# Kernel tuning notes

Measured on AMD Instinct MI355X. Metric: run time of the kernel, lower is better.

The kernel has to match this reference:

```python
import jax, jax.numpy as jnp
import numpy as np

N = 50000
E = 800000
C = 64
NEG_SLOPE = 0.2


def gat_conv(x, edge_index, W, att_src, att_dst, bias, heads, out_ch):
    """PyG GATConv forward (concat=True, add_self_loops=True).
    x: [N, in], edge_index: [2, E] (row0=src j, row1=dst i),
    W: [in, heads*out_ch], att_src/att_dst: [heads, out_ch], bias: [heads*out_ch].
    """
    n = x.shape[0]
    loop = jnp.arange(n, dtype=edge_index.dtype)
    src = jnp.concatenate([edge_index[0], loop])
    dst = jnp.concatenate([edge_index[1], loop])

    xl = (x @ W).reshape(n, heads, out_ch)            # [N, H, F]
    a_src = jnp.einsum('nhf,hf->nh', xl, att_src)      # [N, H]
    a_dst = jnp.einsum('nhf,hf->nh', xl, att_dst)      # [N, H]

    alpha = jax.nn.leaky_relu(a_src[src] + a_dst[dst], NEG_SLOPE)  # [E', H]
    # segment softmax over incoming edges of each destination node
    amax = jax.ops.segment_max(alpha, dst, num_segments=n)
    alpha = jnp.exp(alpha - amax[dst])
    denom = jax.ops.segment_sum(alpha, dst, num_segments=n)
    alpha = alpha / denom[dst]

    # gather source features, weight, scatter-add to destinations
    msg = xl[src] * alpha[:, :, None]                  # [E', H, F]
    out = jax.ops.segment_sum(msg, dst, num_segments=n)  # [N, H, F]
    return out.reshape(n, heads * out_ch) + bias


def setup_inputs() -> dict:
    key = jax.random.key(0)
    ks = jax.random.split(key, 12)
    x = jax.random.normal(ks[0], (N, C), dtype=jnp.float32)
    undirected = jax.random.randint(ks[1], (2, E), 0, N, dtype=jnp.int32)
    directed = jax.random.randint(ks[2], (2, E), 0, N, dtype=jnp.int32)

    s1 = 1.0 / np.sqrt(C)
    s2 = 1.0 / np.sqrt(2 * C)
    W1 = jax.random.normal(ks[3], (C, 2 * C), dtype=jnp.float32) * s1
    att_src1 = jax.random.normal(ks[4], (2, C), dtype=jnp.float32) * s1
    att_dst1 = jax.random.normal(ks[5], (2, C), dtype=jnp.float32) * s1
    b1 = jnp.zeros((2 * C,), dtype=jnp.float32)

    W2 = jax.random.normal(ks[6], (2 * C, 4 * C), dtype=jnp.float32) * s2
    att_src2 = jax.random.normal(ks[7], (2, 2 * C), dtype=jnp.float32) * s2
    att_dst2 = jax.random.normal(ks[8], (2, 2 * C), dtype=jnp.float32) * s2
    b2 = jnp.zeros((4 * C,), dtype=jnp.float32)

    return {
        'x': x,
        'undirected_edges_small': undirected,
        'directed_edges_small': directed,
        'W1': W1, 'att_src1': att_src1, 'att_dst1': att_dst1, 'b1': b1,
        'W2': W2, 'att_src2': att_src2, 'att_dst2': att_dst2, 'b2': b2,
    }


def reference(x, undirected_edges_small, directed_edges_small,
              W1, att_src1, att_dst1, b1,
              W2, att_src2, att_dst2, b2):
    h = gat_conv(x, undirected_edges_small, W1, att_src1, att_dst1, b1,
                 heads=2, out_ch=C)            # [N, 2C]
    out = gat_conv(h, directed_edges_small, W2, att_src2, att_dst2, b2,
                   heads=2, out_ch=2 * C)      # [N, 4C]
    return out
```

## Files before the change

kernel.cpp:

```cpp
#include <hip/hip_runtime.h>
#include <stdint.h>

#define N_NODES 50000
#define N_EDGES 800000
#define CAP 64
#define NBUCK 400
#define BSZ 125
#define BCAP 2816

typedef __attribute__((ext_vector_type(8))) short bf16x8;
typedef __attribute__((ext_vector_type(4))) float f32x4;

__device__ __forceinline__ float b2f_bits(unsigned int lo16) {
    union { unsigned int i; float f; } v; v.i = lo16 << 16; return v.f;
}
__device__ __forceinline__ unsigned short f2b(float f) {
    union { float f; unsigned int i; } v; v.f = f;
    unsigned int x = v.i;
    return (unsigned short)((x + 0x7fffu + ((x >> 16) & 1u)) >> 16);
}
__device__ __forceinline__ void split2(float v, unsigned short& h, unsigned short& l) {
    h = f2b(v);
    l = f2b(v - b2f_bits(h));
}

__global__ __launch_bounds__(256) void proj_kernel(
    const float* __restrict__ W1, const float* __restrict__ as1, const float* __restrict__ ad1,
    const float* __restrict__ b1,
    const float* __restrict__ W2, const float* __restrict__ as2, const float* __restrict__ ad2,
    float* __restrict__ P1, float* __restrict__ q2, float* __restrict__ cs)
{
    __shared__ float p2[4 * 128];
    for (int i = threadIdx.x; i < 4 * 128; i += 256) {
        const int t = i >> 7, c = i & 127;
        const int h = t & 1;
        const float* att = (t < 2) ? as2 : ad2;
        float s = 0.f;
        for (int cc = 0; cc < 128; ++cc)
            s += att[h * 128 + cc] * W2[(size_t)c * 256 + h * 128 + cc];
        p2[i] = s;
    }
    {
        const int t = threadIdx.x >> 6, k = threadIdx.x & 63;
        const int h = t & 1;
        const float* att = (t < 2) ? as1 : ad1;
        float s = 0.f;
        for (int c = 0; c < 64; ++c)
            s += att[h * 64 + c] * W1[(size_t)k * 128 + h * 64 + c];
        P1[t * 64 + k] = s;
    }
    __syncthreads();
    for (int i = threadIdx.x; i < 4 * 128; i += 256) {
        const int t = i >> 7, j = i & 127;
        const int hc = j >> 6, k = j & 63;
        float s = 0.f;
        for (int c = 0; c < 64; ++c)
            s += W1[(size_t)k * 128 + hc * 64 + c] * p2[t * 128 + hc * 64 + c];
        q2[i] = s;
    }
    if (threadIdx.x < 4) {
        const int t = threadIdx.x;
        float s = 0.f;
        for (int c = 0; c < 128; ++c) s += b1[c] * p2[t * 128 + c];
        cs[t] = s;
    }
}

__global__ __launch_bounds__(256) void prep1_kernel(
    const float* __restrict__ X, const float* __restrict__ P1,
    unsigned short* __restrict__ Xh,
    float* __restrict__ a_src, float* __restrict__ a_dst, int n)
{
    const int node = (blockIdx.x * 256 + threadIdx.x) >> 4;
    const int sl = threadIdx.x & 15;
    if (node >= n) return;
    const float4 v = *(const float4*)(X + (size_t)node * 64 + sl * 4);
    ushort4 hv;
    hv.x = f2b(v.x); hv.y = f2b(v.y); hv.z = f2b(v.z); hv.w = f2b(v.w);
    *(ushort4*)(Xh + (size_t)node * 64 + sl * 4) = hv;
    float d[4];
#pragma unroll
    for (int t = 0; t < 4; ++t) {
        const float* pp = P1 + t * 64 + sl * 4;
        d[t] = v.x * pp[0] + v.y * pp[1] + v.z * pp[2] + v.w * pp[3];
    }
#pragma unroll
    for (int o = 1; o < 16; o <<= 1)
#pragma unroll
        for (int t = 0; t < 4; ++t) d[t] += __shfl_xor(d[t], o);
    if (sl == 0) {
        *(float2*)(a_src + node * 2) = make_float2(d[0], d[1]);
        *(float2*)(a_dst + node * 2) = make_float2(d[2], d[3]);
    }
}

__global__ __launch_bounds__(256) void splitWT_kernel(
    const float* __restrict__ W,
    unsigned short* __restrict__ WhT, unsigned short* __restrict__ WlT, int K, int N)
{
    const int i = blockIdx.x * 256 + threadIdx.x;
    if (i >= N * K) return;
    const int n = i / K, k = i % K;
    const float v = W[(size_t)k * N + n];
    unsigned short h, l;
    split2(v, h, l);
    WhT[i] = h; WlT[i] = l;
}

__global__ __launch_bounds__(256) void bucket_kernel(
    const int* __restrict__ e1, const int* __restrict__ e2, int ne,
    int* __restrict__ gcur, unsigned int* __restrict__ stage)
{
    const int layer = blockIdx.x & 1;
    const int bslot = blockIdx.x >> 1;
    const int nbl = gridDim.x >> 1;
    const int* __restrict__ eix = layer ? e2 : e1;
    int* cur = gcur + layer * NBUCK;
    unsigned int* __restrict__ stg = stage + (size_t)layer * NBUCK * BCAP;

    __shared__ int cnt_lds[NBUCK];
    __shared__ int base_lds[NBUCK];
    constexpr int EPT = 16;
    constexpr int CHUNK = 256 * EPT;

    for (int base = bslot * CHUNK; base < ne; base += nbl * CHUNK) {
        for (int i = threadIdx.x; i < NBUCK; i += 256) cnt_lds[i] = 0;
        __syncthreads();

        unsigned int rec[EPT];
        int bk[EPT];
#pragma unroll
        for (int i = 0; i < EPT; ++i) {
            const int e = base + i * 256 + threadIdx.x;
            bk[i] = -1;
            if (e < ne) {
                const int s = eix[e];
                const int d = eix[ne + e];
                if ((unsigned)d < (unsigned)N_NODES) {
                    const int b = d / BSZ;
                    bk[i] = b;
                    rec[i] = (unsigned)s | ((unsigned)(d - b * BSZ) << 16);
                    atomicAdd(&cnt_lds[b], 1);
                }
            }
        }
        __syncthreads();
        for (int i = threadIdx.x; i < NBUCK; i += 256) {
            const int c = cnt_lds[i];
            base_lds[i] = c ? atomicAdd(&cur[i], c) : 0;
            cnt_lds[i] = 0;
        }
        __syncthreads();
#pragma unroll
        for (int i = 0; i < EPT; ++i) {
            if (bk[i] >= 0) {
                const int idx = base_lds[bk[i]] + atomicAdd(&cnt_lds[bk[i]], 1);
                if (idx < BCAP) stg[(size_t)bk[i] * BCAP + idx] = rec[i];
            }
        }
        __syncthreads();
    }
}

__global__ __launch_bounds__(256) void place_kernel(
    const unsigned int* __restrict__ stage, const int* __restrict__ gcur,
    int* __restrict__ cnt1, int* __restrict__ cnt2,
    int* __restrict__ ss1, int* __restrict__ ss2)
{
    const int layer = blockIdx.x & 1;
    const int bucket = blockIdx.x >> 1;
    int m = gcur[layer * NBUCK + bucket];
    m = m < BCAP ? m : BCAP;
    const unsigned int* __restrict__ stg =
        stage + ((size_t)(layer * NBUCK + bucket)) * BCAP;
    int* __restrict__ cnt = layer ? cnt2 : cnt1;
    int* __restrict__ ss  = layer ? ss2 : ss1;
    const int d0 = bucket * BSZ;

    __shared__ int c_lds[BSZ];
    __shared__ __align__(16) unsigned int img[BSZ * CAP];

    for (int i = threadIdx.x; i < BSZ; i += 256) c_lds[i] = 0;
    __syncthreads();

    for (int i = threadIdx.x; i < m; i += 256) {
        const unsigned int v = stg[i];
        const int dr = (int)(v >> 16);
        const int slot = atomicAdd(&c_lds[dr], 1);
        if (slot < CAP) img[dr * CAP + slot] = v & 0xffffu;
    }
    __syncthreads();

    uint4* dst4 = (uint4*)(ss + (size_t)d0 * CAP);
    const uint4* src4 = (const uint4*)img;
    constexpr int NV4 = BSZ * CAP / 4;
    for (int i = threadIdx.x; i < NV4; i += 256) dst4[i] = src4[i];
    for (int i = threadIdx.x; i < BSZ; i += 256) {
        const int c = c_lds[i];
        cnt[d0 + i] = c < CAP ? c : CAP;
    }
}

__global__ __launch_bounds__(256) void agg1_kernel(
    const unsigned short* __restrict__ XH, const float* __restrict__ X,
    const float* __restrict__ a_src, const float* __restrict__ a_dst,
    const int* __restrict__ cnt, const int* __restrict__ bins,
    unsigned short* __restrict__ AH, unsigned short* __restrict__ AL, int n)
{
    const int node = (blockIdx.x * 256 + threadIdx.x) >> 6;
    const int lane = threadIdx.x & 63;
    if (node >= n) return;
    const int hl = lane & 15;
    const int sub = lane >> 4;

    const int s = node * CAP;
    int deg = cnt[node]; deg = deg < CAP ? deg : CAP;
    const int e = s + deg;
    const float2 ad = *(const float2*)(a_dst + node * 2);

    float acc0[4] = {0.f, 0.f, 0.f, 0.f}, acc1[4] = {0.f, 0.f, 0.f, 0.f};
    float den0 = 0.f, den1 = 0.f;

    int p = s;
    for (; p + 8 <= e; p += 8) {
        int j[2];
        j[0] = bins[p + sub];
        j[1] = bins[p + 4 + sub];
        float2 A[2];
        A[0] = *(const float2*)(a_src + j[0] * 2);
        A[1] = *(const float2*)(a_src + j[1] * 2);
        uint2 u[2];
        u[0] = *(const uint2*)(XH + (size_t)j[0] * 64 + hl * 4);
        u[1] = *(const uint2*)(XH + (size_t)j[1] * 64 + hl * 4);
#pragma unroll
        for (int g = 0; g < 2; ++g) {
            float l0 = A[g].x + ad.x; l0 = l0 > 0.f ? l0 : 0.2f * l0;
            float l1 = A[g].y + ad.y; l1 = l1 > 0.f ? l1 : 0.2f * l1;
            const float w0 = __expf(l0), w1 = __expf(l1);
            den0 += w0; den1 += w1;
            float f[4];
            f[0] = b2f_bits(u[g].x & 0xffffu); f[1] = b2f_bits(u[g].x >> 16);
            f[2] = b2f_bits(u[g].y & 0xffffu); f[3] = b2f_bits(u[g].y >> 16);
#pragma unroll
            for (int k = 0; k < 4; ++k) { acc0[k] += w0 * f[k]; acc1[k] += w1 * f[k]; }
        }
    }
    for (; p < e; p += 4) {
        const int pos = p + sub;
        const int pc = pos < e ? pos : e - 1;
        const int j = bins[pc];
        const float2 A = *(const float2*)(a_src + j * 2);
        const uint2 u = *(const uint2*)(XH + (size_t)j * 64 + hl * 4);
        float l0 = A.x + ad.x; l0 = l0 > 0.f ? l0 : 0.2f * l0;
        float l1 = A.y + ad.y; l1 = l1 > 0.f ? l1 : 0.2f * l1;
        float w0 = __expf(l0), w1 = __expf(l1);
        if (pos >= e) { w0 = 0.f; w1 = 0.f; }
        den0 += w0; den1 += w1;
        float f[4];
        f[0] = b2f_bits(u.x & 0xffffu); f[1] = b2f_bits(u.x >> 16);
        f[2] = b2f_bits(u.y & 0xffffu); f[3] = b2f_bits(u.y >> 16);
#pragma unroll
        for (int k = 0; k < 4; ++k) { acc0[k] += w0 * f[k]; acc1[k] += w1 * f[k]; }
    }
    if (sub == 0) {
        const float2 A = *(const float2*)(a_src + node * 2);
        const float4 v = *(const float4*)(X + (size_t)node * 64 + hl * 4);
        float l0 = A.x + ad.x; l0 = l0 > 0.f ? l0 : 0.2f * l0;
        float l1 = A.y + ad.y; l1 = l1 > 0.f ? l1 : 0.2f * l1;
        const float w0 = __expf(l0), w1 = __expf(l1);
        den0 += w0; den1 += w1;
        acc0[0] += w0 * v.x; acc0[1] += w0 * v.y; acc0[2] += w0 * v.z; acc0[3] += w0 * v.w;
        acc1[0] += w1 * v.x; acc1[1] += w1 * v.y; acc1[2] += w1 * v.z; acc1[3] += w1 * v.w;
    }
#pragma unroll
    for (int o = 16; o < 64; o <<= 1) {
        den0 += __shfl_xor(den0, o); den1 += __shfl_xor(den1, o);
#pragma unroll
        for (int k = 0; k < 4; ++k) {
            acc0[k] += __shfl_xor(acc0[k], o);
            acc1[k] += __shfl_xor(acc1[k], o);
        }
    }
    if (lane < 32) {
        const int head = lane >> 4;
        float vv[4];
        if (head) {
            const float inv = 1.f / den1;
            vv[0] = acc1[0] * inv; vv[1] = acc1[1] * inv;
            vv[2] = acc1[2] * inv; vv[3] = acc1[3] * inv;
        } else {
            const float inv = 1.f / den0;
            vv[0] = acc0[0] * inv; vv[1] = acc0[1] * inv;
            vv[2] = acc0[2] * inv; vv[3] = acc0[3] * inv;
        }
        ushort4 hv, lv;
        split2(vv[0], hv.x, lv.x); split2(vv[1], hv.y, lv.y);
        split2(vv[2], hv.z, lv.z); split2(vv[3], hv.w, lv.w);
        const size_t off = (size_t)head * N_NODES * 64 + (size_t)node * 64 + hl * 4;
        *(ushort4*)(AH + off) = hv;
        *(ushort4*)(AL + off) = lv;
    }
}

__global__ __launch_bounds__(256) void att2_kernel(
    const unsigned short* __restrict__ A1H, const unsigned short* __restrict__ A1L,
    const float* __restrict__ q2, const float* __restrict__ cs,
    float* __restrict__ a_src, float* __restrict__ a_dst, int n)
{
    const int node = (blockIdx.x * 256 + threadIdx.x) >> 6;
    const int lane = threadIdx.x & 63;
    if (node >= n) return;
    const int hc = lane >> 5;
    const int k2 = (lane & 31) * 2;
    const size_t off = (size_t)hc * N_NODES * 64 + (size_t)node * 64 + k2;
    const unsigned int uh = *(const unsigned int*)(A1H + off);
    const unsigned int ul = *(const unsigned int*)(A1L + off);
    const float v0 = b2f_bits(uh & 0xffffu) + b2f_bits(ul & 0xffffu);
    const float v1 = b2f_bits(uh >> 16) + b2f_bits(ul >> 16);
    const int j = hc * 64 + k2;
    float d[4];
#pragma unroll
    for (int t = 0; t < 4; ++t)
        d[t] = v0 * q2[t * 128 + j] + v1 * q2[t * 128 + j + 1];
#pragma unroll
    for (int o = 1; o < 64; o <<= 1)
#pragma unroll
        for (int t = 0; t < 4; ++t) d[t] += __shfl_xor(d[t], o);
    if (lane == 0) {
        *(float2*)(a_src + node * 2) = make_float2(d[0] + cs[0], d[1] + cs[1]);
        *(float2*)(a_dst + node * 2) = make_float2(d[2] + cs[2], d[3] + cs[3]);
    }
}

__global__ __launch_bounds__(256) void agg2_kernel(
    const unsigned short* __restrict__ HH, const unsigned short* __restrict__ HL,
    const float* __restrict__ a_src, const float* __restrict__ a_dst,
    const int* __restrict__ cnt, const int* __restrict__ bins,
    unsigned short* __restrict__ AH, unsigned short* __restrict__ AL, int n)
{
    const int node = (blockIdx.x * 256 + threadIdx.x) >> 6;
    const int lane = threadIdx.x & 63;
    if (node >= n) return;
    const int hl = lane & 31;
    const int sub = lane >> 5;

    const int s = node * CAP;
    int deg = cnt[node]; deg = deg < CAP ? deg : CAP;
    const int e = s + deg;
    const float2 ad = *(const float2*)(a_dst + node * 2);

    float acc0[4] = {0.f, 0.f, 0.f, 0.f}, acc1[4] = {0.f, 0.f, 0.f, 0.f};
    float den0 = 0.f, den1 = 0.f;

    int p = s;
    for (; p + 8 <= e; p += 8) {
        int j[4];
#pragma unroll
        for (int g = 0; g < 4; ++g) j[g] = bins[p + g * 2 + sub];
        float2 A[4];
#pragma unroll
        for (int g = 0; g < 4; ++g) A[g] = *(const float2*)(a_src + j[g] * 2);
        uint2 u[4];
#pragma unroll
        for (int g = 0; g < 4; ++g)
            u[g] = *(const uint2*)(HH + (size_t)j[g] * 128 + hl * 4);
#pragma unroll
        for (int g = 0; g < 4; ++g) {
            float l0 = A[g].x + ad.x; l0 = l0 > 0.f ? l0 : 0.2f * l0;
            float l1 = A[g].y + ad.y; l1 = l1 > 0.f ? l1 : 0.2f * l1;
            const float w0 = __expf(l0), w1 = __expf(l1);
            den0 += w0; den1 += w1;
            float f[4];
            f[0] = b2f_bits(u[g].x & 0xffffu); f[1] = b2f_bits(u[g].x >> 16);
            f[2] = b2f_bits(u[g].y & 0xffffu); f[3] = b2f_bits(u[g].y >> 16);
#pragma unroll
            for (int k = 0; k < 4; ++k) { acc0[k] += w0 * f[k]; acc1[k] += w1 * f[k]; }
        }
    }
    for (; p < e; p += 2) {
        const int pos = p + sub;
        const int pc = pos < e ? pos : e - 1;
        const int j = bins[pc];
        const float2 A = *(const float2*)(a_src + j * 2);
        const uint2 u = *(const uint2*)(HH + (size_t)j * 128 + hl * 4);
        float l0 = A.x + ad.x; l0 = l0 > 0.f ? l0 : 0.2f * l0;
        float l1 = A.y + ad.y; l1 = l1 > 0.f ? l1 : 0.2f * l1;
        float w0 = __expf(l0), w1 = __expf(l1);
        if (pos >= e) { w0 = 0.f; w1 = 0.f; }
        den0 += w0; den1 += w1;
        float f[4];
        f[0] = b2f_bits(u.x & 0xffffu); f[1] = b2f_bits(u.x >> 16);
        f[2] = b2f_bits(u.y & 0xffffu); f[3] = b2f_bits(u.y >> 16);
#pragma unroll
        for (int k = 0; k < 4; ++k) { acc0[k] += w0 * f[k]; acc1[k] += w1 * f[k]; }
    }
    if (sub == 0) {
        const float2 A = *(const float2*)(a_src + node * 2);
        const uint2 uh = *(const uint2*)(HH + (size_t)node * 128 + hl * 4);
        const uint2 ul = *(const uint2*)(HL + (size_t)node * 128 + hl * 4);
        float l0 = A.x + ad.x; l0 = l0 > 0.f ? l0 : 0.2f * l0;
        float l1 = A.y + ad.y; l1 = l1 > 0.f ? l1 : 0.2f * l1;
        const float w0 = __expf(l0), w1 = __expf(l1);
        den0 += w0; den1 += w1;
        float f[4];
        f[0] = b2f_bits(uh.x & 0xffffu) + b2f_bits(ul.x & 0xffffu);
        f[1] = b2f_bits(uh.x >> 16) + b2f_bits(ul.x >> 16);
        f[2] = b2f_bits(uh.y & 0xffffu) + b2f_bits(ul.y & 0xffffu);
        f[3] = b2f_bits(uh.y >> 16) + b2f_bits(ul.y >> 16);
#pragma unroll
        for (int k = 0; k < 4; ++k) { acc0[k] += w0 * f[k]; acc1[k] += w1 * f[k]; }
    }
    den0 += __shfl_xor(den0, 32); den1 += __shfl_xor(den1, 32);
#pragma unroll
    for (int k = 0; k < 4; ++k) {
        acc0[k] += __shfl_xor(acc0[k], 32);
        acc1[k] += __shfl_xor(acc1[k], 32);
    }
    {
        const int head = sub;
        float vv[4];
        if (head) {
            const float inv = 1.f / den1;
            vv[0] = acc1[0] * inv; vv[1] = acc1[1] * inv;
            vv[2] = acc1[2] * inv; vv[3] = acc1[3] * inv;
        } else {
            const float inv = 1.f / den0;
            vv[0] = acc0[0] * inv; vv[1] = acc0[1] * inv;
            vv[2] = acc0[2] * inv; vv[3] = acc0[3] * inv;
        }
        ushort4 hv, lv;
        split2(vv[0], hv.x, lv.x); split2(vv[1], hv.y, lv.y);
        split2(vv[2], hv.z, lv.z); split2(vv[3], hv.w, lv.w);
        const size_t off = (size_t)head * N_NODES * 128 + (size_t)node * 128 + hl * 4;
        *(ushort4*)(AH + off) = hv;
        *(ushort4*)(AL + off) = lv;
    }
}

__global__ __launch_bounds__(512) void gemm_h_kernel(
    const unsigned short* __restrict__ AH, const unsigned short* __restrict__ AL,
    const unsigned short* __restrict__ WTh, const unsigned short* __restrict__ WTl,
    const float* __restrict__ b1,
    unsigned short* __restrict__ HH, unsigned short* __restrict__ HL, int M)
{
    constexpr int K = 64, KC = 2;
    const int wave = threadIdx.x >> 6;
    const int lane = threadIdx.x & 63;
    const int head = wave >> 2;
    const int c0 = (wave & 3) * 16;
    const int lr = lane & 15;
    const int lk = (lane >> 4) * 8;
    const int colg = head * 64 + c0 + ((lane >> 4) << 2);

    bf16x8 awh[KC], awl[KC];
    {
        const unsigned short* wr  = WTh + (size_t)(head * 64 + c0 + lr) * K + lk;
        const unsigned short* wr2 = WTl + (size_t)(head * 64 + c0 + lr) * K + lk;
#pragma unroll
        for (int c = 0; c < KC; ++c) {
            awh[c] = *(const bf16x8*)(wr + c * 32);
            awl[c] = *(const bf16x8*)(wr2 + c * 32);
        }
    }
    const float4 bias = *(const float4*)(b1 + colg);
    const unsigned short* XhB = AH + (size_t)head * M * 64;
    const unsigned short* XlB = AL + (size_t)head * M * 64;

    auto loadB = [&](bf16x8 (&bh)[KC], bf16x8 (&bl)[KC], int sidx) {
        const unsigned short* xr  = XhB + (size_t)(sidx * 16 + lr) * 64 + lk;
        const unsigned short* xr2 = XlB + (size_t)(sidx * 16 + lr) * 64 + lk;
#pragma unroll
        for (int c = 0; c < KC; ++c) {
            bh[c] = *(const bf16x8*)(xr + c * 32);
            bl[c] = *(const bf16x8*)(xr2 + c * 32);
        }
    };
    auto compute = [&](bf16x8 (&bh)[KC], bf16x8 (&bl)[KC], int sidx) {
        f32x4 acc = {0.f, 0.f, 0.f, 0.f};
#pragma unroll
        for (int c = 0; c < KC; ++c)
            acc = __builtin_amdgcn_mfma_f32_16x16x32_bf16(awh[c], bh[c], acc, 0, 0, 0);
#pragma unroll
        for (int c = 0; c < KC; ++c)
            acc = __builtin_amdgcn_mfma_f32_16x16x32_bf16(awh[c], bl[c], acc, 0, 0, 0);
#pragma unroll
        for (int c = 0; c < KC; ++c)
            acc = __builtin_amdgcn_mfma_f32_16x16x32_bf16(awl[c], bh[c], acc, 0, 0, 0);
        ushort4 hv, lv;
        split2(acc[0] + bias.x, hv.x, lv.x); split2(acc[1] + bias.y, hv.y, lv.y);
        split2(acc[2] + bias.z, hv.z, lv.z); split2(acc[3] + bias.w, hv.w, lv.w);
        const size_t o = (size_t)(sidx * 16 + lr) * 128 + colg;
        *(ushort4*)(HH + o) = hv;
        *(ushort4*)(HL + o) = lv;
    };

    const int NSTRIP = M / 16;
    const int nb = gridDim.x;
    int s = blockIdx.x;
    bf16x8 b0h[KC], b0l[KC], b1h_[KC], b1l_[KC];
    if (s < NSTRIP) loadB(b0h, b0l, s);
    while (s < NSTRIP) {
        const int sn = s + nb;
        if (sn < NSTRIP) loadB(b1h_, b1l_, sn);
        compute(b0h, b0l, s);
        if (sn >= NSTRIP) break;
        const int sn2 = sn + nb;
        if (sn2 < NSTRIP) loadB(b0h, b0l, sn2);
        compute(b1h_, b1l_, sn);
        s = sn2;
    }
}

__global__ __launch_bounds__(512) void gemm_out_kernel(
    const unsigned short* __restrict__ AH, const unsigned short* __restrict__ AL,
    const unsigned short* __restrict__ WTh, const unsigned short* __restrict__ WTl,
    const float* __restrict__ b2,
    float* __restrict__ OUT, int M)
{
    constexpr int K = 128, KC = 4, CT = 2;
    const int wave = threadIdx.x >> 6;
    const int lane = threadIdx.x & 63;
    const int head = wave >> 2;
    const int c0 = (wave & 3) * 32;
    const int lr = lane & 15;
    const int lk = (lane >> 4) * 8;

    bf16x8 awh[CT][KC], awl[CT][KC];
    float4 bias[CT];
    int colg[CT];
#pragma unroll
    for (int t = 0; t < CT; ++t) {
        const unsigned short* wr  = WTh + (size_t)(head * 128 + c0 + t * 16 + lr) * K + lk;
        const unsigned short* wr2 = WTl + (size_t)(head * 128 + c0 + t * 16 + lr) * K + lk;
#pragma unroll
        for (int c = 0; c < KC; ++c) {
            awh[t][c] = *(const bf16x8*)(wr + c * 32);
            awl[t][c] = *(const bf16x8*)(wr2 + c * 32);
        }
        colg[t] = head * 128 + c0 + t * 16 + ((lane >> 4) << 2);
        bias[t] = *(const float4*)(b2 + colg[t]);
    }
    const unsigned short* XhB = AH + (size_t)head * M * 128;
    const unsigned short* XlB = AL + (size_t)head * M * 128;

    auto loadB = [&](bf16x8 (&bh)[KC], bf16x8 (&bl)[KC], int sidx) {
        const unsigned short* xr  = XhB + (size_t)(sidx * 16 + lr) * 128 + lk;
        const unsigned short* xr2 = XlB + (size_t)(sidx * 16 + lr) * 128 + lk;
#pragma unroll
        for (int c = 0; c < KC; ++c) {
            bh[c] = *(const bf16x8*)(xr + c * 32);
            bl[c] = *(const bf16x8*)(xr2 + c * 32);
        }
    };
    auto compute = [&](bf16x8 (&bh)[KC], bf16x8 (&bl)[KC], int sidx) {
#pragma unroll
        for (int t = 0; t < CT; ++t) {
            f32x4 acc = {0.f, 0.f, 0.f, 0.f};
#pragma unroll
            for (int c = 0; c < KC; ++c)
                acc = __builtin_amdgcn_mfma_f32_16x16x32_bf16(awh[t][c], bh[c], acc, 0, 0, 0);
#pragma unroll
            for (int c = 0; c < KC; ++c)
                acc = __builtin_amdgcn_mfma_f32_16x16x32_bf16(awh[t][c], bl[c], acc, 0, 0, 0);
#pragma unroll
            for (int c = 0; c < KC; ++c)
                acc = __builtin_amdgcn_mfma_f32_16x16x32_bf16(awl[t][c], bh[c], acc, 0, 0, 0);
            float4 o;
            o.x = acc[0] + bias[t].x; o.y = acc[1] + bias[t].y;
            o.z = acc[2] + bias[t].z; o.w = acc[3] + bias[t].w;
            *(float4*)(OUT + (size_t)(sidx * 16 + lr) * 256 + colg[t]) = o;
        }
    };

    const int NSTRIP = M / 16;
    const int nb = gridDim.x;
    int s = blockIdx.x;
    bf16x8 b0h[KC], b0l[KC], b1h_[KC], b1l_[KC];
    if (s < NSTRIP) loadB(b0h, b0l, s);
    while (s < NSTRIP) {
        const int sn = s + nb;
        if (sn < NSTRIP) loadB(b1h_, b1l_, sn);
        compute(b0h, b0l, s);
        if (sn >= NSTRIP) break;
        const int sn2 = sn + nb;
        if (sn2 < NSTRIP) loadB(b0h, b0l, sn2);
        compute(b1h_, b1l_, sn);
        s = sn2;
    }
}

extern "C" void kernel_launch(void* const* d_in, const int* in_sizes, int n_in,
                              void* d_out, int out_size, void* d_ws, size_t ws_size,
                              hipStream_t stream)
{
    const int N = N_NODES, E = N_EDGES;

    const float* x   = (const float*)d_in[0];
    const int*   und = (const int*)d_in[1];
    const int*   dir = (const int*)d_in[2];
    const float* W1  = (const float*)d_in[3];
    const float* as1 = (const float*)d_in[4];
    const float* ad1 = (const float*)d_in[5];
    const float* b1  = (const float*)d_in[6];
    const float* W2  = (const float*)d_in[7];
    const float* as2 = (const float*)d_in[8];
    const float* ad2 = (const float*)d_in[9];
    const float* b2  = (const float*)d_in[10];

    char* p = (char*)d_ws;
    auto alloc = [&](size_t bytes) {
        char* r = p;
        p += (bytes + 255) & ~(size_t)255;
        return r;
    };
    unsigned short* agg2h = (unsigned short*)alloc((size_t)2 * N * 128 * 2);
    unsigned short* agg2l = (unsigned short*)alloc((size_t)2 * N * 128 * 2);
    unsigned short* hlbuf = (unsigned short*)alloc((size_t)N * 128 * 2);
    int*   ss1   = (int*)alloc((size_t)N * CAP * 4);
    int*   ss2   = (int*)alloc((size_t)N * CAP * 4);
    float* a_src1 = (float*)alloc((size_t)N * 2 * 4);
    float* a_dst1 = (float*)alloc((size_t)N * 2 * 4);
    float* a_src2 = (float*)alloc((size_t)N * 2 * 4);
    float* a_dst2 = (float*)alloc((size_t)N * 2 * 4);
    int*   cnts  = (int*)alloc(((size_t)2 * N + 2 * NBUCK) * 4);
    unsigned short* w1th = (unsigned short*)alloc((size_t)128 * 64 * 2);
    unsigned short* w1tl = (unsigned short*)alloc((size_t)128 * 64 * 2);
    unsigned short* w2th = (unsigned short*)alloc((size_t)256 * 128 * 2);
    unsigned short* w2tl = (unsigned short*)alloc((size_t)256 * 128 * 2);
    float* P1d = (float*)alloc(4 * 64 * 4);
    float* q2d = (float*)alloc(4 * 128 * 4);
    float* csd = (float*)alloc(4 * 4);
    int* cnt1 = cnts, * cnt2 = cnts + N, * gcur = cnts + 2 * N;

    unsigned int* stage = (unsigned int*)agg2h;
    unsigned short* hhbuf = (unsigned short*)ss1;
    unsigned short* x1h   = (unsigned short*)d_out;
    unsigned short* agg1h = (unsigned short*)d_out + (size_t)N * 64;
    unsigned short* agg1l = (unsigned short*)d_out + (size_t)N * 64 + (size_t)N * 128;

    const int WB = (N * 64) / 256;

    proj_kernel<<<1, 256, 0, stream>>>(W1, as1, ad1, b1, W2, as2, ad2, P1d, q2d, csd);
    hipMemsetAsync(gcur, 0, (size_t)2 * NBUCK * 4, stream);
    bucket_kernel<<<2 * 196, 256, 0, stream>>>(und, dir, E, gcur, stage);
    place_kernel<<<2 * NBUCK, 256, 0, stream>>>(stage, gcur, cnt1, cnt2, ss1, ss2);
    prep1_kernel<<<(N * 16) / 256, 256, 0, stream>>>(x, P1d, x1h, a_src1, a_dst1, N);
    splitWT_kernel<<<(128 * 64 + 255) / 256, 256, 0, stream>>>(W1, w1th, w1tl, 64, 128);
    splitWT_kernel<<<(256 * 128 + 255) / 256, 256, 0, stream>>>(W2, w2th, w2tl, 128, 256);

    agg1_kernel<<<WB, 256, 0, stream>>>(x1h, x, a_src1, a_dst1, cnt1, ss1, agg1h, agg1l, N);
    gemm_h_kernel<<<768, 512, 0, stream>>>(agg1h, agg1l, w1th, w1tl, b1, hhbuf, hlbuf, N);
    att2_kernel<<<WB, 256, 0, stream>>>(agg1h, agg1l, q2d, csd, a_src2, a_dst2, N);

    agg2_kernel<<<WB, 256, 0, stream>>>(hhbuf, hlbuf, a_src2, a_dst2, cnt2, ss2, agg2h, agg2l, N);
    gemm_out_kernel<<<512, 512, 0, stream>>>(agg2h, agg2l, w2th, w2tl, b2, (float*)d_out, N);
}
```

Before: 297.1 us.

## Fuse layer-2 attention logits into gemm_h, widen aggregation loads, merge W prep

The separate att2_kernel is removed. The layer-2 attention projections are now computed inside gemm_h_kernel from the A tiles already held in registers, and accumulated into a zeroed buffer with atomicAdd. The cs constant is folded into the a_dst term in agg2. Both aggregation kernels switch from 8-byte to 16-byte gather loads with 8 features per lane and drop the unrolled main loop. The two weight-split kernels are merged into one launch. The changes aim to cut a full pass over agg1 and a launch, at the cost of atomics, an extra memset and more register pressure in the GEMM.

```diff
diff --git a/kernel.cpp b/kernel.cpp
--- a/kernel.cpp
+++ b/kernel.cpp
@@ -22,6 +22,21 @@
 __device__ __forceinline__ void split2(float v, unsigned short& h, unsigned short& l) {
     h = f2b(v);
     l = f2b(v - b2f_bits(h));
+}
+__device__ __forceinline__ void unpack8(const uint4 u, float* f) {
+    f[0] = b2f_bits(u.x & 0xffffu); f[1] = b2f_bits(u.x >> 16);
+    f[2] = b2f_bits(u.y & 0xffffu); f[3] = b2f_bits(u.y >> 16);
+    f[4] = b2f_bits(u.z & 0xffffu); f[5] = b2f_bits(u.z >> 16);
+    f[6] = b2f_bits(u.w & 0xffffu); f[7] = b2f_bits(u.w >> 16);
+}
+__device__ __forceinline__ void pack8hl(const float* v, uint4& H, uint4& L) {
+    unsigned short h[8], l[8];
+#pragma unroll
+    for (int k = 0; k < 8; ++k) split2(v[k], h[k], l[k]);
+    H.x = h[0] | ((unsigned)h[1] << 16); H.y = h[2] | ((unsigned)h[3] << 16);
+    H.z = h[4] | ((unsigned)h[5] << 16); H.w = h[6] | ((unsigned)h[7] << 16);
+    L.x = l[0] | ((unsigned)l[1] << 16); L.y = l[2] | ((unsigned)l[3] << 16);
+    L.z = l[4] | ((unsigned)l[5] << 16); L.w = l[6] | ((unsigned)l[7] << 16);
 }
 
 __global__ __launch_bounds__(256) void proj_kernel(
@@ -94,17 +109,25 @@
     }
 }
 
-__global__ __launch_bounds__(256) void splitWT_kernel(
-    const float* __restrict__ W,
-    unsigned short* __restrict__ WhT, unsigned short* __restrict__ WlT, int K, int N)
-{
-    const int i = blockIdx.x * 256 + threadIdx.x;
-    if (i >= N * K) return;
-    const int n = i / K, k = i % K;
-    const float v = W[(size_t)k * N + n];
-    unsigned short h, l;
-    split2(v, h, l);
-    WhT[i] = h; WlT[i] = l;
+__global__ __launch_bounds__(256) void prepW_kernel(
+    const float* __restrict__ W1, const float* __restrict__ W2,
+    unsigned short* __restrict__ w1h, unsigned short* __restrict__ w1l,
+    unsigned short* __restrict__ w2h, unsigned short* __restrict__ w2l)
+{
+    const int bid = blockIdx.x;
+    if (bid < 128) {
+        const int i = bid * 256 + threadIdx.x;
+        const int n = i >> 7, k = i & 127;
+        unsigned short h, l;
+        split2(W2[(size_t)k * 256 + n], h, l);
+        w2h[i] = h; w2l[i] = l;
+    } else {
+        const int i = (bid - 128) * 256 + threadIdx.x;
+        const int n = i >> 6, k = i & 63;
+        unsigned short h, l;
+        split2(W1[(size_t)k * 128 + n], h, l);
+        w1h[i] = h; w1l[i] = l;
+    }
 }
 
 __global__ __launch_bounds__(256) void bucket_kernel(
@@ -210,238 +233,154 @@
     const int node = (blockIdx.x * 256 + threadIdx.x) >> 6;
     const int lane = threadIdx.x & 63;
     if (node >= n) return;
-    const int hl = lane & 15;
-    const int sub = lane >> 4;
+    const int hl = lane & 7;
+    const int sub = lane >> 3;
 
     const int s = node * CAP;
     int deg = cnt[node]; deg = deg < CAP ? deg : CAP;
     const int e = s + deg;
     const float2 ad = *(const float2*)(a_dst + node * 2);
 
-    float acc0[4] = {0.f, 0.f, 0.f, 0.f}, acc1[4] = {0.f, 0.f, 0.f, 0.f};
+    float acc0[8] = {0.f,0.f,0.f,0.f,0.f,0.f,0.f,0.f};
+    float acc1[8] = {0.f,0.f,0.f,0.f,0.f,0.f,0.f,0.f};
     float den0 = 0.f, den1 = 0.f;
 
-    int p = s;
-    for (; p + 8 <= e; p += 8) {
-        int j[2];
-        j[0] = bins[p + sub];
-        j[1] = bins[p + 4 + sub];
-        float2 A[2];
-        A[0] = *(const float2*)(a_src + j[0] * 2);
-        A[1] = *(const float2*)(a_src + j[1] * 2);
-        uint2 u[2];
-        u[0] = *(const uint2*)(XH + (size_t)j[0] * 64 + hl * 4);
-        u[1] = *(const uint2*)(XH + (size_t)j[1] * 64 + hl * 4);
-#pragma unroll
-        for (int g = 0; g < 2; ++g) {
-            float l0 = A[g].x + ad.x; l0 = l0 > 0.f ? l0 : 0.2f * l0;
-            float l1 = A[g].y + ad.y; l1 = l1 > 0.f ? l1 : 0.2f * l1;
-            const float w0 = __expf(l0), w1 = __expf(l1);
-            den0 += w0; den1 += w1;
-            float f[4];
-            f[0] = b2f_bits(u[g].x & 0xffffu); f[1] = b2f_bits(u[g].x >> 16);
-            f[2] = b2f_bits(u[g].y & 0xffffu); f[3] = b2f_bits(u[g].y >> 16);
-#pragma unroll
-            for (int k = 0; k < 4; ++k) { acc0[k] += w0 * f[k]; acc1[k] += w1 * f[k]; }
-        }
-    }
-    for (; p < e; p += 4) {
+    for (int p = s; p < e; p += 8) {
         const int pos = p + sub;
         const int pc = pos < e ? pos : e - 1;
         const int j = bins[pc];
         const float2 A = *(const float2*)(a_src + j * 2);
-        const uint2 u = *(const uint2*)(XH + (size_t)j * 64 + hl * 4);
+        const uint4 u = *(const uint4*)(XH + (size_t)j * 64 + hl * 8);
         float l0 = A.x + ad.x; l0 = l0 > 0.f ? l0 : 0.2f * l0;
         float l1 = A.y + ad.y; l1 = l1 > 0.f ? l1 : 0.2f * l1;
         float w0 = __expf(l0), w1 = __expf(l1);
         if (pos >= e) { w0 = 0.f; w1 = 0.f; }
         den0 += w0; den1 += w1;
-        float f[4];
-        f[0] = b2f_bits(u.x & 0xffffu); f[1] = b2f_bits(u.x >> 16);
-        f[2] = b2f_bits(u.y & 0xffffu); f[3] = b2f_bits(u.y >> 16);
-#pragma unroll
-        for (int k = 0; k < 4; ++k) { acc0[k] += w0 * f[k]; acc1[k] += w1 * f[k]; }
+        float f[8]; unpack8(u, f);
+#pragma unroll
+        for (int k = 0; k < 8; ++k) { acc0[k] += w0 * f[k]; acc1[k] += w1 * f[k]; }
     }
     if (sub == 0) {
         const float2 A = *(const float2*)(a_src + node * 2);
-        const float4 v = *(const float4*)(X + (size_t)node * 64 + hl * 4);
+        const float4 va = *(const float4*)(X + (size_t)node * 64 + hl * 8);
+        const float4 vb = *(const float4*)(X + (size_t)node * 64 + hl * 8 + 4);
         float l0 = A.x + ad.x; l0 = l0 > 0.f ? l0 : 0.2f * l0;
         float l1 = A.y + ad.y; l1 = l1 > 0.f ? l1 : 0.2f * l1;
         const float w0 = __expf(l0), w1 = __expf(l1);
         den0 += w0; den1 += w1;
-        acc0[0] += w0 * v.x; acc0[1] += w0 * v.y; acc0[2] += w0 * v.z; acc0[3] += w0 * v.w;
-        acc1[0] += w1 * v.x; acc1[1] += w1 * v.y; acc1[2] += w1 * v.z; acc1[3] += w1 * v.w;
-    }
-#pragma unroll
-    for (int o = 16; o < 64; o <<= 1) {
+        float f[8] = {va.x, va.y, va.z, va.w, vb.x, vb.y, vb.z, vb.w};
+#pragma unroll
+        for (int k = 0; k < 8; ++k) { acc0[k] += w0 * f[k]; acc1[k] += w1 * f[k]; }
+    }
+#pragma unroll
+    for (int o = 8; o < 64; o <<= 1) {
         den0 += __shfl_xor(den0, o); den1 += __shfl_xor(den1, o);
 #pragma unroll
-        for (int k = 0; k < 4; ++k) {
+        for (int k = 0; k < 8; ++k) {
             acc0[k] += __shfl_xor(acc0[k], o);
             acc1[k] += __shfl_xor(acc1[k], o);
         }
     }
-    if (lane < 32) {
-        const int head = lane >> 4;
-        float vv[4];
-        if (head) {
-            const float inv = 1.f / den1;
-            vv[0] = acc1[0] * inv; vv[1] = acc1[1] * inv;
-            vv[2] = acc1[2] * inv; vv[3] = acc1[3] * inv;
-        } else {
-            const float inv = 1.f / den0;
-            vv[0] = acc0[0] * inv; vv[1] = acc0[1] * inv;
-            vv[2] = acc0[2] * inv; vv[3] = acc0[3] * inv;
-        }
-        ushort4 hv, lv;
-        split2(vv[0], hv.x, lv.x); split2(vv[1], hv.y, lv.y);
-        split2(vv[2], hv.z, lv.z); split2(vv[3], hv.w, lv.w);
-        const size_t off = (size_t)head * N_NODES * 64 + (size_t)node * 64 + hl * 4;
-        *(ushort4*)(AH + off) = hv;
-        *(ushort4*)(AL + off) = lv;
-    }
-}
-
-__global__ __launch_bounds__(256) void att2_kernel(
-    const unsigned short* __restrict__ A1H, const unsigned short* __restrict__ A1L,
-    const float* __restrict__ q2, const float* __restrict__ cs,
-    float* __restrict__ a_src, float* __restrict__ a_dst, int n)
+    if (sub < 2) {
+        const int head = sub;
+        const float inv = 1.f / (head ? den1 : den0);
+        float vv[8];
+#pragma unroll
+        for (int k = 0; k < 8; ++k) vv[k] = (head ? acc1[k] : acc0[k]) * inv;
+        uint4 H, L;
+        pack8hl(vv, H, L);
+        const size_t off = (size_t)head * N_NODES * 64 + (size_t)node * 64 + hl * 8;
+        *(uint4*)(AH + off) = H;
+        *(uint4*)(AL + off) = L;
+    }
+}
+
+__global__ __launch_bounds__(256) void agg2_kernel(
+    const unsigned short* __restrict__ HH, const unsigned short* __restrict__ HL,
+    const float* __restrict__ a_src, const float* __restrict__ a_dst,
+    const float* __restrict__ cs,
+    const int* __restrict__ cnt, const int* __restrict__ bins,
+    unsigned short* __restrict__ AH, unsigned short* __restrict__ AL, int n)
 {
     const int node = (blockIdx.x * 256 + threadIdx.x) >> 6;
     const int lane = threadIdx.x & 63;
     if (node >= n) return;
-    const int hc = lane >> 5;
-    const int k2 = (lane & 31) * 2;
-    const size_t off = (size_t)hc * N_NODES * 64 + (size_t)node * 64 + k2;
-    const unsigned int uh = *(const unsigned int*)(A1H + off);
-    const unsigned int ul = *(const unsigned int*)(A1L + off);
-    const float v0 = b2f_bits(uh & 0xffffu) + b2f_bits(ul & 0xffffu);
-    const float v1 = b2f_bits(uh >> 16) + b2f_bits(ul >> 16);
-    const int j = hc * 64 + k2;
-    float d[4];
-#pragma unroll
-    for (int t = 0; t < 4; ++t)
-        d[t] = v0 * q2[t * 128 + j] + v1 * q2[t * 128 + j + 1];
-#pragma unroll
-    for (int o = 1; o < 64; o <<= 1)
-#pragma unroll
-        for (int t = 0; t < 4; ++t) d[t] += __shfl_xor(d[t], o);
-    if (lane == 0) {
-        *(float2*)(a_src + node * 2) = make_float2(d[0] + cs[0], d[1] + cs[1]);
-        *(float2*)(a_dst + node * 2) = make_float2(d[2] + cs[2], d[3] + cs[3]);
-    }
-}
-
-__global__ __launch_bounds__(256) void agg2_kernel(
-    const unsigned short* __restrict__ HH, const unsigned short* __restrict__ HL,
-    const float* __restrict__ a_src, const float* __restrict__ a_dst,
-    const int* __restrict__ cnt, const int* __restrict__ bins,
-    unsigned short* __restrict__ AH, unsigned short* __restrict__ AL, int n)
-{
-    const int node = (blockIdx.x * 256 + threadIdx.x) >> 6;
-    const int lane = threadIdx.x & 63;
-    if (node >= n) return;
-    const int hl = lane & 31;
-    const int sub = lane >> 5;
+    const int hl = lane & 15;
+    const int sub = lane >> 4;
+
+    const float4 csv = *(const float4*)cs;
+    const float C0 = csv.x + csv.z, C1 = csv.y + csv.w;
 
     const int s = node * CAP;
     int deg = cnt[node]; deg = deg < CAP ? deg : CAP;
     const int e = s + deg;
     const float2 ad = *(const float2*)(a_dst + node * 2);
-
-    float acc0[4] = {0.f, 0.f, 0.f, 0.f}, acc1[4] = {0.f, 0.f, 0.f, 0.f};
+    const float ad0 = ad.x + C0, ad1 = ad.y + C1;
+
+    float acc0[8] = {0.f,0.f,0.f,0.f,0.f,0.f,0.f,0.f};
+    float acc1[8] = {0.f,0.f,0.f,0.f,0.f,0.f,0.f,0.f};
     float den0 = 0.f, den1 = 0.f;
 
-    int p = s;
-    for (; p + 8 <= e; p += 8) {
-        int j[4];
-#pragma unroll
-        for (int g = 0; g < 4; ++g) j[g] = bins[p + g * 2 + sub];
-        float2 A[4];
-#pragma unroll
-        for (int g = 0; g < 4; ++g) A[g] = *(const float2*)(a_src + j[g] * 2);
-        uint2 u[4];
-#pragma unroll
-        for (int g = 0; g < 4; ++g)
-            u[g] = *(const uint2*)(HH + (size_t)j[g] * 128 + hl * 4);
-#pragma unroll
-        for (int g = 0; g < 4; ++g) {
-            float l0 = A[g].x + ad.x; l0 = l0 > 0.f ? l0 : 0.2f * l0;
-            float l1 = A[g].y + ad.y; l1 = l1 > 0.f ? l1 : 0.2f * l1;
-            const float w0 = __expf(l0), w1 = __expf(l1);
-            den0 += w0; den1 += w1;
-            float f[4];
-            f[0] = b2f_bits(u[g].x & 0xffffu); f[1] = b2f_bits(u[g].x >> 16);
-            f[2] = b2f_bits(u[g].y & 0xffffu); f[3] = b2f_bits(u[g].y >> 16);
-#pragma unroll
-            for (int k = 0; k < 4; ++k) { acc0[k] += w0 * f[k]; acc1[k] += w1 * f[k]; }
-        }
-    }
-    for (; p < e; p += 2) {
+    for (int p = s; p < e; p += 4) {
         const int pos = p + sub;
         const int pc = pos < e ? pos : e - 1;
         const int j = bins[pc];
         const float2 A = *(const float2*)(a_src + j * 2);
-        const uint2 u = *(const uint2*)(HH + (size_t)j * 128 + hl * 4);
-        float l0 = A.x + ad.x; l0 = l0 > 0.f ? l0 : 0.2f * l0;
-        float l1 = A.y + ad.y; l1 = l1 > 0.f ? l1 : 0.2f * l1;
+        const uint4 u = *(const uint4*)(HH + (size_t)j * 128 + hl * 8);
+        float l0 = A.x + ad0; l0 = l0 > 0.f ? l0 : 0.2f * l0;
+        float l1 = A.y + ad1; l1 = l1 > 0.f ? l1 : 0.2f * l1;
         float w0 = __expf(l0), w1 = __expf(l1);
         if (pos >= e) { w0 = 0.f; w1 = 0.f; }
         den0 += w0; den1 += w1;
-        float f[4];
-        f[0] = b2f_bits(u.x & 0xffffu); f[1] = b2f_bits(u.x >> 16);
-        f[2] = b2f_bits(u.y & 0xffffu); f[3] = b2f_bits(u.y >> 16);
-#pragma unroll
-        for (int k = 0; k < 4; ++k) { acc0[k] += w0 * f[k]; acc1[k] += w1 * f[k]; }
+        float f[8]; unpack8(u, f);
+#pragma unroll
+        for (int k = 0; k < 8; ++k) { acc0[k] += w0 * f[k]; acc1[k] += w1 * f[k]; }
     }
     if (sub == 0) {
         const float2 A = *(const float2*)(a_src + node * 2);
-        const uint2 uh = *(const uint2*)(HH + (size_t)node * 128 + hl * 4);
-        const uint2 ul = *(const uint2*)(HL + (size_t)node * 128 + hl * 4);
-        float l0 = A.x + ad.x; l0 = l0 > 0.f ? l0 : 0.2f * l0;
-        float l1 = A.y + ad.y; l1 = l1 > 0.f ? l1 : 0.2f * l1;
+        const uint4 uh = *(const uint4*)(HH + (size_t)node * 128 + hl * 8);
+        const uint4 ul = *(const uint4*)(HL + (size_t)node * 128 + hl * 8);
+        float l0 = A.x + ad0; l0 = l0 > 0.f ? l0 : 0.2f * l0;
+        float l1 = A.y + ad1; l1 = l1 > 0.f ? l1 : 0.2f * l1;
         const float w0 = __expf(l0), w1 = __expf(l1);
         den0 += w0; den1 += w1;
-        float f[4];
-        f[0] = b2f_bits(uh.x & 0xffffu) + b2f_bits(ul.x & 0xffffu);
-        f[1] = b2f_bits(uh.x >> 16) + b2f_bits(ul.x >> 16);
-        f[2] = b2f_bits(uh.y & 0xffffu) + b2f_bits(ul.y & 0xffffu);
-        f[3] = b2f_bits(uh.y >> 16) + b2f_bits(ul.y >> 16);
-#pragma unroll
-        for (int k = 0; k < 4; ++k) { acc0[k] += w0 * f[k]; acc1[k] += w1 * f[k]; }
-    }
-    den0 += __shfl_xor(den0, 32); den1 += __shfl_xor(den1, 32);
-#pragma unroll
-    for (int k = 0; k < 4; ++k) {
-        acc0[k] += __shfl_xor(acc0[k], 32);
-        acc1[k] += __shfl_xor(acc1[k], 32);
-    }
-    {
+        float fh[8], fl[8];
+        unpack8(uh, fh); unpack8(ul, fl);
+#pragma unroll
+        for (int k = 0; k < 8; ++k) {
+            const float f = fh[k] + fl[k];
+            acc0[k] += w0 * f; acc1[k] += w1 * f;
+        }
+    }
+#pragma unroll
+    for (int o = 16; o < 64; o <<= 1) {
+        den0 += __shfl_xor(den0, o); den1 += __shfl_xor(den1, o);
+#pragma unroll
+        for (int k = 0; k < 8; ++k) {
+            acc0[k] += __shfl_xor(acc0[k], o);
+            acc1[k] += __shfl_xor(acc1[k], o);
+        }
+    }
+    if (sub < 2) {
         const int head = sub;
-        float vv[4];
-        if (head) {
-            const float inv = 1.f / den1;
-            vv[0] = acc1[0] * inv; vv[1] = acc1[1] * inv;
-            vv[2] = acc1[2] * inv; vv[3] = acc1[3] * inv;
-        } else {
-            const float inv = 1.f / den0;
-            vv[0] = acc0[0] * inv; vv[1] = acc0[1] * inv;
-            vv[2] = acc0[2] * inv; vv[3] = acc0[3] * inv;
-        }
-        ushort4 hv, lv;
-        split2(vv[0], hv.x, lv.x); split2(vv[1], hv.y, lv.y);
-        split2(vv[2], hv.z, lv.z); split2(vv[3], hv.w, lv.w);
-        const size_t off = (size_t)head * N_NODES * 128 + (size_t)node * 128 + hl * 4;
-        *(ushort4*)(AH + off) = hv;
-        *(ushort4*)(AL + off) = lv;
+        const float inv = 1.f / (head ? den1 : den0);
+        float vv[8];
+#pragma unroll
+        for (int k = 0; k < 8; ++k) vv[k] = (head ? acc1[k] : acc0[k]) * inv;
+        uint4 H, L;
+        pack8hl(vv, H, L);
+        const size_t off = (size_t)head * N_NODES * 128 + (size_t)node * 128 + hl * 8;
+        *(uint4*)(AH + off) = H;
+        *(uint4*)(AL + off) = L;
     }
 }
 
 __global__ __launch_bounds__(512) void gemm_h_kernel(
     const unsigned short* __restrict__ AH, const unsigned short* __restrict__ AL,
     const unsigned short* __restrict__ WTh, const unsigned short* __restrict__ WTl,
-    const float* __restrict__ b1,
-    unsigned short* __restrict__ HH, unsigned short* __restrict__ HL, int M)
+    const float* __restrict__ b1, const float* __restrict__ q2,
+    unsigned short* __restrict__ HH, unsigned short* __restrict__ HL,
+    float* __restrict__ a_src2, float* __restrict__ a_dst2, int M)
 {
     constexpr int K = 64, KC = 2;
     const int wave = threadIdx.x >> 6;
@@ -451,6 +390,7 @@
     const int lr = lane & 15;
     const int lk = (lane >> 4) * 8;
     const int colg = head * 64 + c0 + ((lane >> 4) << 2);
+    const bool doAtt = (wave & 3) == 0;
 
     bf16x8 awh[KC], awl[KC];
     {
@@ -492,6 +432,30 @@
         const size_t o = (size_t)(sidx * 16 + lr) * 128 + colg;
         *(ushort4*)(HH + o) = hv;
         *(ushort4*)(HL + o) = lv;
+        if (doAtt) {
+            float P[4] = {0.f, 0.f, 0.f, 0.f};
+#pragma unroll
+            for (int c = 0; c < KC; ++c)
+#pragma unroll
+                for (int i = 0; i < 8; ++i) {
+                    const float v = b2f_bits((unsigned short)bh[c][i])
+                                  + b2f_bits((unsigned short)bl[c][i]);
+                    const int kk = head * 64 + lk + c * 32 + i;
+#pragma unroll
+                    for (int t = 0; t < 4; ++t) P[t] += v * q2[t * 128 + kk];
+                }
+#pragma unroll
+            for (int o2 = 16; o2 < 64; o2 <<= 1)
+#pragma unroll
+                for (int t = 0; t < 4; ++t) P[t] += __shfl_xor(P[t], o2);
+            if (lane < 16) {
+                const int m = sidx * 16 + lane;
+                atomicAdd(&a_src2[m * 2 + 0], P[0]);
+                atomicAdd(&a_src2[m * 2 + 1], P[1]);
+                atomicAdd(&a_dst2[m * 2 + 0], P[2]);
+                atomicAdd(&a_dst2[m * 2 + 1], P[3]);
+            }
+        }
     };
 
     const int NSTRIP = M / 16;
@@ -620,8 +584,7 @@
     int*   ss2   = (int*)alloc((size_t)N * CAP * 4);
     float* a_src1 = (float*)alloc((size_t)N * 2 * 4);
     float* a_dst1 = (float*)alloc((size_t)N * 2 * 4);
-    float* a_src2 = (float*)alloc((size_t)N * 2 * 4);
-    float* a_dst2 = (float*)alloc((size_t)N * 2 * 4);
+    float* att2buf = (float*)alloc((size_t)N * 4 * 4);
     int*   cnts  = (int*)alloc(((size_t)2 * N + 2 * NBUCK) * 4);
     unsigned short* w1th = (unsigned short*)alloc((size_t)128 * 64 * 2);
     unsigned short* w1tl = (unsigned short*)alloc((size_t)128 * 64 * 2);
@@ -631,6 +594,7 @@
     float* q2d = (float*)alloc(4 * 128 * 4);
     float* csd = (float*)alloc(4 * 4);
     int* cnt1 = cnts, * cnt2 = cnts + N, * gcur = cnts + 2 * N;
+    float* a_src2 = att2buf, * a_dst2 = att2buf + (size_t)N * 2;
 
     unsigned int* stage = (unsigned int*)agg2h;
     unsigned short* hhbuf = (unsigned short*)ss1;
@@ -642,16 +606,17 @@
 
     proj_kernel<<<1, 256, 0, stream>>>(W1, as1, ad1, b1, W2, as2, ad2, P1d, q2d, csd);
     hipMemsetAsync(gcur, 0, (size_t)2 * NBUCK * 4, stream);
+    hipMemsetAsync(att2buf, 0, (size_t)N * 4 * 4, stream);
     bucket_kernel<<<2 * 196, 256, 0, stream>>>(und, dir, E, gcur, stage);
     place_kernel<<<2 * NBUCK, 256, 0, stream>>>(stage, gcur, cnt1, cnt2, ss1, ss2);
     prep1_kernel<<<(N * 16) / 256, 256, 0, stream>>>(x, P1d, x1h, a_src1, a_dst1, N);
-    splitWT_kernel<<<(128 * 64 + 255) / 256, 256, 0, stream>>>(W1, w1th, w1tl, 64, 128);
-    splitWT_kernel<<<(256 * 128 + 255) / 256, 256, 0, stream>>>(W2, w2th, w2tl, 128, 256);
+    prepW_kernel<<<160, 256, 0, stream>>>(W1, W2, w1th, w1tl, w2th, w2tl);
 
     agg1_kernel<<<WB, 256, 0, stream>>>(x1h, x, a_src1, a_dst1, cnt1, ss1, agg1h, agg1l, N);
-    gemm_h_kernel<<<768, 512, 0, stream>>>(agg1h, agg1l, w1th, w1tl, b1, hhbuf, hlbuf, N);
-    att2_kernel<<<WB, 256, 0, stream>>>(agg1h, agg1l, q2d, csd, a_src2, a_dst2, N);
-
-    agg2_kernel<<<WB, 256, 0, stream>>>(hhbuf, hlbuf, a_src2, a_dst2, cnt2, ss2, agg2h, agg2l, N);
+    gemm_h_kernel<<<768, 512, 0, stream>>>(agg1h, agg1l, w1th, w1tl, b1, q2d,
+                                           hhbuf, hlbuf, a_src2, a_dst2, N);
+
+    agg2_kernel<<<WB, 256, 0, stream>>>(hhbuf, hlbuf, a_src2, a_dst2, csd,
+                                        cnt2, ss2, agg2h, agg2l, N);
     gemm_out_kernel<<<512, 512, 0, stream>>>(agg2h, agg2l, w2th, w2tl, b2, (float*)d_out, N);
 }
```

New measurement: 292.6 us. Within noise of the previous version (-1.5%).
